# Performance work log

Measured on AMD Instinct MI355X. Metric: run time of the kernel, lower is better.

Reference implementation:

```python
import jax, jax.numpy as jnp
import numpy as np

K = 3          # kernel_size (forced by hardcoded padding=1 in query unfold)
PAD = 1        # padding
C_IN = 64      # conv in_channels (x has C_IN + 5 channels)
C_OUT = 128    # out_channels
B, H, W = 16, 32, 32


def unfold(x, k, pad=0, mode='constant'):
    """torch.nn.functional.unfold equivalent. x: (B,C,H,W) -> (B, C*k*k, L).
    Ordering matches torch: channel slowest, then kernel row, then kernel col."""
    if pad:
        x = jnp.pad(x, ((0, 0), (0, 0), (pad, pad), (pad, pad)), mode=mode)
    b, c, h, w = x.shape
    oh, ow = h - k + 1, w - k + 1
    # (B, C, k*k, oh, ow) with patch index i*k+j
    patches = jnp.stack([x[:, :, i:i + oh, j:j + ow]
                         for i in range(k) for j in range(k)], axis=2)
    return patches.reshape(b, c * k * k, oh * ow)


def conv2d(x, w, b, pad):
    out = jax.lax.conv_general_dilated(
        x, w, window_strides=(1, 1), padding=[(pad, pad), (pad, pad)],
        dimension_numbers=('NCHW', 'OIHW', 'NCHW'))
    return out + b[None, :, None, None]


def setup_inputs() -> dict:
    key = jax.random.key(0)
    ks = jax.random.split(key, 6)
    fan1 = C_IN * K * K
    fan2 = C_OUT * 1 * 1
    return {
        'x': jax.random.normal(ks[0], (B, C_IN + 5, H, W), jnp.float32),
        'conv_w': jax.random.normal(ks[1], (C_OUT, C_IN, K, K), jnp.float32) / np.sqrt(fan1),
        'conv_b': jax.random.normal(ks[2], (C_OUT,), jnp.float32) * 0.01,
        'conv2_w': jax.random.normal(ks[3], (1, C_OUT, 1, 1), jnp.float32) / np.sqrt(fan2),
        'conv2_b': jax.random.normal(ks[4], (1,), jnp.float32) * 0.01,
        'shapes_kernel': jax.random.uniform(ks[5], (1, C_OUT, K * K * 5, 1), jnp.float32),
    }


def reference(x, conv_w, conv_b, conv2_w, conv2_b, shapes_kernel):
    k, pad = K, PAD
    center = k * k // 2

    conv_out = conv2d(x[:, :-5], conv_w, conv_b, pad)          # (B, C_OUT, H', W')
    b, cout, oh, ow = conv_out.shape
    L = oh * ow

    # shape-channel windows (replication-padded), center-relative positions
    sw = unfold(x[:, -5:], k, pad, 'edge').reshape(b, 5, k * k, L)
    sw = sw.at[:, 0:2].add(-sw[:, 0:2, center:center + 1])

    # L1 distance of each window to each learned shape kernel
    sd = jnp.abs(sw.reshape(b, 1, 5 * k * k, L) - shapes_kernel).sum(axis=2)  # (B, C_OUT, L)
    sd = sd.reshape(b, cout, oh, ow)

    saf = jax.nn.relu(conv_out / (sd + 1.0))                    # shape_attended_features

    q = conv2d(saf, conv2_w, conv2_b, 0) / jnp.sqrt(jnp.float32(cout))  # (B, 1, H', W')
    qu = jax.nn.softmax(unfold(q, k, 1), axis=1)[:, None]       # (B, 1, k*k, L), zero-padded

    u_mean = unfold(x[:, -5:-3], k, pad, 'edge').reshape(b, 2, k * k, L)
    means = (u_mean * qu).sum(axis=2)                           # (B, 2, L)

    v1 = (unfold(x[:, -3:-1], k, pad, 'edge').reshape(b, 2, k * k, L) * qu).sum(axis=2)
    v2 = (((u_mean - means[:, :, None, :]) ** 2) * qu).sum(axis=2)
    var = v1 + v2                                               # (B, 2, L)

    c1 = (unfold(x[:, -1:], k, pad, 'edge').reshape(b, 1, k * k, L) * qu).sum(axis=2)
    c2 = ((u_mean[:, 0:1] - means[:, 0:1, None, :]) *
          (u_mean[:, 1:2] - means[:, 1:2, None, :]) * qu).sum(axis=2)
    covar = c1 + c2                                             # (B, 1, L)

    agg = jnp.concatenate([means, var, covar], axis=1).reshape(b, 5, oh, ow)
    return jnp.concatenate([saf, agg], axis=1)                  # (B, C_OUT+5, H', W')
```

## Files before the change

### kernel.cpp

```cpp
#include <hip/hip_runtime.h>
#include <math.h>

#define CI 64
#define CO 128
#define CX 69
#define LPIX 1024

typedef __attribute__((ext_vector_type(8))) short bf16x8;
typedef __attribute__((ext_vector_type(4))) float f32x4;

#define WMF_OFF  0
#define QP_OFF   147456

__device__ __forceinline__ unsigned short f2bf(float f) {
  unsigned u = __float_as_uint(f);
  unsigned r = (u + 0x7fffu + ((u >> 16) & 1u)) >> 16;
  return (unsigned short)r;
}

__launch_bounds__(256)
__global__ void prepW(const float* __restrict__ cwg,
                      unsigned short* __restrict__ wmf) {
  int i = blockIdx.x * 256 + threadIdx.x;
  if (i < 128 * 9 * 64) {
    int co = i / 576, rem = i - co * 576;
    int tap = rem >> 6, ci = rem & 63;
    wmf[i] = f2bf(cwg[co * 576 + ci * 9 + tap]);
  }
}

__launch_bounds__(512, 4)
__global__ void convFused(const float* __restrict__ xg,
                          const unsigned short* __restrict__ wmfg,
                          const float* __restrict__ cbg,
                          const float* __restrict__ w2g,
                          const float* __restrict__ skg,
                          float* __restrict__ qp,
                          float* __restrict__ outg) {
  __shared__ char arena[18432];
  __shared__ float lds_sx[5 * 144];
  __shared__ float qred[8][64];

  unsigned short* ldsB = (unsigned short*)arena;
  float* lds_c = (float*)arena;

  const int tid = threadIdx.x;
  const int blk = blockIdx.x;
  const int coh = blk & 1;
  const int rp  = (blk >> 1) & 15;
  const int b   = blk >> 5;
  const int r0  = rp * 2;

  const int w    = tid >> 6;
  const int lane = tid & 63;
  const int rsel = w >> 2;
  const int ct   = w & 3;
  const int n16  = lane & 15;
  const int kq   = lane >> 4;

  const float* xb = xg + (size_t)b * CX * LPIX;
  const float* xs = xb + CI * LPIX;

  bf16x8 areg[2][9];
  {
    const unsigned short* abase =
        wmfg + (size_t)(coh * 64 + ct * 16 + n16) * 576 + kq * 8;
    #pragma unroll
    for (int ch = 0; ch < 2; ++ch)
      #pragma unroll
      for (int tap = 0; tap < 9; ++tap)
        areg[ch][tap] = *(const bf16x8*)(abase + tap * 64 + ch * 32);
  }

  {
    const int row  = tid >> 7;
    const int cip  = (tid >> 2) & 31;
    const int colq = tid & 3;
    const int ci   = cip * 2;
    const int c0   = colq * 8;
    const int grow = r0 - 1 + row;
    f32x4 u0a = {}, u0b = {}, u1a = {}, u1b = {};
    if ((unsigned)grow < 32u) {
      const float* p0 = xb + ci * LPIX + grow * 32 + c0;
      u0a = *(const f32x4*)p0;          u0b = *(const f32x4*)(p0 + 4);
      u1a = *(const f32x4*)(p0 + LPIX); u1b = *(const f32x4*)(p0 + LPIX + 4);
    }
    #pragma unroll
    for (int cc = 0; cc < 8; ++cc) {
      float f0 = (cc < 4) ? u0a[cc] : u0b[cc - 4];
      float f1 = (cc < 4) ? u1a[cc] : u1b[cc - 4];
      unsigned v = (unsigned)f2bf(f0) | ((unsigned)f2bf(f1) << 16);
      const int slot  = c0 + cc + 1;
      const int gslot = ((ci >> 3) << 3) ^ ((slot & 7) << 3);
      ((unsigned*)ldsB)[(((row * 36 + slot) << 6) + gslot + (ci & 7)) >> 1] = v;
    }
    {
      const int prw = tid >> 7;
      const int s4  = (tid >> 5) & 3;
      const int sl  = (s4 == 0) ? 0 : (32 + s4);
      const int ci2 = (tid & 31) * 2;
      const int gsl = ((ci2 >> 3) << 3) ^ ((sl & 7) << 3);
      ((unsigned*)ldsB)[(((prw * 36 + sl) << 6) + gsl + (ci2 & 7)) >> 1] = 0;
    }
  }

  for (int idx = tid; idx < 5 * 144; idx += 512) {
    int c = idx / 144, rem = idx - c * 144;
    int s = rem / 36, j = rem - s * 36;
    int hh = r0 - 1 + s; hh = hh < 0 ? 0 : (hh > 31 ? 31 : hh);
    int col = j - 1;     col = col < 0 ? 0 : (col > 31 ? 31 : col);
    lds_sx[idx] = xs[c * LPIX + hh * 32 + col];
  }
  __syncthreads();

  f32x4 acc[2] = {};
  #pragma unroll
  for (int tap = 0; tap < 9; ++tap) {
    const int dr = tap / 3, dc = tap % 3;
    const int rowst = rsel + dr;
    #pragma unroll
    for (int ch = 0; ch < 2; ++ch) {
      const int g = (ch << 2) + kq;
      #pragma unroll
      for (int pt = 0; pt < 2; ++pt) {
        const int slot = pt * 16 + n16 + dc;
        const int gs = (g ^ (slot & 7)) << 3;
        bf16x8 bfr = *(const bf16x8*)(ldsB + ((rowst * 36 + slot) << 6) + gs);
        acc[pt] = __builtin_amdgcn_mfma_f32_16x16x32_bf16(areg[ch][tap], bfr,
                                                          acc[pt], 0, 0, 0);
      }
    }
  }
  __syncthreads();

  #pragma unroll
  for (int pt = 0; pt < 2; ++pt) {
    const int pxl = rsel * 32 + pt * 16 + n16;
    const int cog = ct * 4 + kq;
    const int sg  = cog ^ (pxl & 7);
    *(f32x4*)&lds_c[pxl * 64 + sg * 4] = acc[pt];
  }
  __syncthreads();

  const int wS   = __builtin_amdgcn_readfirstlane(w);
  const int co0g = coh * 64 + wS * 8;
  const int pxl  = lane;

  float cvals[8];
  #pragma unroll
  for (int g = 0; g < 2; ++g) {
    const int cog = wS * 2 + g;
    const int sg  = cog ^ (pxl & 7);
    *(f32x4*)&cvals[g * 4] = *(const f32x4*)&lds_c[pxl * 64 + sg * 4];
  }

  const int xbase = (pxl >> 5) * 36 + (pxl & 31);
  float swv[45];
  {
    const float c0 = lds_sx[0 * 144 + 37 + xbase];
    const float c1 = lds_sx[1 * 144 + 37 + xbase];
    #pragma unroll
    for (int c = 0; c < 5; ++c) {
      float ctr = (c == 0) ? c0 : ((c == 1) ? c1 : 0.f);
      #pragma unroll
      for (int s = 0; s < 3; ++s)
        #pragma unroll
        for (int dc = 0; dc < 3; ++dc)
          swv[c * 9 + s * 3 + dc] = lds_sx[c * 144 + s * 36 + dc + xbase] - ctr;
    }
  }

  float sd[8];
  #pragma unroll
  for (int k = 0; k < 8; ++k) {
    const float* kp = skg + (size_t)(co0g + k) * 45;
    float s = 0.f;
    #pragma unroll
    for (int j = 0; j < 45; ++j)
      s += fabsf(swv[j] - kp[j]);
    sd[k] = s;
  }

  float qpv = 0.f;
  float* ob = outg + ((size_t)b * 133 + co0g) * LPIX + (r0 + (pxl >> 5)) * 32 + (pxl & 31);
  #pragma unroll
  for (int k = 0; k < 8; ++k) {
    float v = (cvals[k] + cbg[co0g + k]) * __builtin_amdgcn_rcpf(sd[k] + 1.0f);
    v = v > 0.f ? v : 0.f;
    ob[(size_t)k * LPIX] = v;
    qpv = fmaf(v, w2g[co0g + k], qpv);
  }

  qred[w][lane] = qpv;
  __syncthreads();
  if (tid < 64) {
    float q = 0.f;
    #pragma unroll
    for (int w8 = 0; w8 < 8; ++w8) q += qred[w8][tid];
    qp[coh * 16384 + b * LPIX + r0 * 32 + tid] = q;
  }
}

__launch_bounds__(64)
__global__ void statsB(const float* __restrict__ xg,
                       const float* __restrict__ qp,
                       const float* __restrict__ b2g,
                       float* __restrict__ outg) {
  const int gid = blockIdx.x * 64 + threadIdx.x;
  const int b = gid >> 10;
  const int h = (gid >> 5) & 31;
  const int w = gid & 31;

  const float b2 = b2g[0];
  const float* q0 = qp + (size_t)b * LPIX;
  float qv[9];
  float m = -1e30f;
  #pragma unroll
  for (int t = 0; t < 9; ++t) {
    int hh = h + t / 3 - 1, wc = w + t % 3 - 1;
    float v = 0.f;
    if ((unsigned)hh < 32u && (unsigned)wc < 32u) {
      int off = hh * 32 + wc;
      v = (q0[off] + q0[16384 + off] + b2) * 0.08838834764831845f;
    }
    qv[t] = v;
    m = fmaxf(m, v);
  }
  float ssum = 0.f;
  #pragma unroll
  for (int t = 0; t < 9; ++t) { qv[t] = expf(qv[t] - m); ssum += qv[t]; }
  const float inv = 1.f / ssum;

  const float* xs = xg + ((size_t)b * CX + CI) * LPIX;
  float um0[9], um1[9];
  float m0 = 0.f, m1 = 0.f, v1a = 0.f, v1b = 0.f, c1 = 0.f;
  #pragma unroll
  for (int t = 0; t < 9; ++t) {
    int hh = h + t / 3 - 1; hh = hh < 0 ? 0 : (hh > 31 ? 31 : hh);
    int wc = w + t % 3 - 1; wc = wc < 0 ? 0 : (wc > 31 ? 31 : wc);
    int off = hh * 32 + wc;
    float quv = qv[t] * inv;
    qv[t] = quv;
    float a0 = xs[off];
    float a1 = xs[LPIX + off];
    float b0 = xs[2 * LPIX + off];
    float b1 = xs[3 * LPIX + off];
    float cc = xs[4 * LPIX + off];
    um0[t] = a0; um1[t] = a1;
    m0 = fmaf(a0, quv, m0);
    m1 = fmaf(a1, quv, m1);
    v1a = fmaf(b0, quv, v1a);
    v1b = fmaf(b1, quv, v1b);
    c1 = fmaf(cc, quv, c1);
  }
  float var0 = v1a, var1 = v1b, cov = c1;
  #pragma unroll
  for (int t = 0; t < 9; ++t) {
    float d0 = um0[t] - m0, d1 = um1[t] - m1;
    var0 = fmaf(d0 * d0, qv[t], var0);
    var1 = fmaf(d1 * d1, qv[t], var1);
    cov  = fmaf(d0 * d1, qv[t], cov);
  }
  float* ob = outg + ((size_t)b * 133 + 128) * LPIX + h * 32 + w;
  ob[0 * LPIX] = m0;
  ob[1 * LPIX] = m1;
  ob[2 * LPIX] = var0;
  ob[3 * LPIX] = var1;
  ob[4 * LPIX] = cov;
}

extern "C" void kernel_launch(void* const* d_in, const int* in_sizes, int n_in,
                              void* d_out, int out_size, void* d_ws, size_t ws_size,
                              hipStream_t stream) {
  const float* x  = (const float*)d_in[0];
  const float* cw = (const float*)d_in[1];
  const float* cb = (const float*)d_in[2];
  const float* w2 = (const float*)d_in[3];
  const float* b2 = (const float*)d_in[4];
  const float* sk = (const float*)d_in[5];
  float* out = (float*)d_out;

  unsigned short* wmf = (unsigned short*)((char*)d_ws + WMF_OFF);
  float* qp = (float*)((char*)d_ws + QP_OFF);

  prepW<<<dim3(576), dim3(256), 0, stream>>>(cw, wmf);
  convFused<<<dim3(512), dim3(512), 0, stream>>>(x, wmf, cb, w2, sk, qp, out);
  statsB<<<dim3(256), dim3(64), 0, stream>>>(x, qp, b2, out);
}
```

Baseline: 29.64 us.

## Compute all output channels per block in fused conv with 1024 threads

```diff
diff --git a/kernel.cpp b/kernel.cpp
--- a/kernel.cpp
+++ b/kernel.cpp
@@ -29,7 +29,7 @@
   }
 }
 
-__launch_bounds__(512, 4)
+__launch_bounds__(1024, 4)
 __global__ void convFused(const float* __restrict__ xg,
                           const unsigned short* __restrict__ wmfg,
                           const float* __restrict__ cbg,
@@ -37,24 +37,23 @@
                           const float* __restrict__ skg,
                           float* __restrict__ qp,
                           float* __restrict__ outg) {
-  __shared__ char arena[18432];
+  __shared__ char arena[32768];
   __shared__ float lds_sx[5 * 144];
-  __shared__ float qred[8][64];
+  __shared__ float qred[16][64];
 
   unsigned short* ldsB = (unsigned short*)arena;
   float* lds_c = (float*)arena;
 
   const int tid = threadIdx.x;
   const int blk = blockIdx.x;
-  const int coh = blk & 1;
-  const int rp  = (blk >> 1) & 15;
-  const int b   = blk >> 5;
+  const int rp  = blk & 15;
+  const int b   = blk >> 4;
   const int r0  = rp * 2;
 
   const int w    = tid >> 6;
   const int lane = tid & 63;
-  const int rsel = w >> 2;
-  const int ct   = w & 3;
+  const int rsel = w >> 3;
+  const int ct   = w & 7;
   const int n16  = lane & 15;
   const int kq   = lane >> 4;
 
@@ -64,7 +63,7 @@
   bf16x8 areg[2][9];
   {
     const unsigned short* abase =
-        wmfg + (size_t)(coh * 64 + ct * 16 + n16) * 576 + kq * 8;
+        wmfg + (size_t)(ct * 16 + n16) * 576 + kq * 8;
     #pragma unroll
     for (int ch = 0; ch < 2; ++ch)
       #pragma unroll
@@ -73,28 +72,27 @@
   }
 
   {
-    const int row  = tid >> 7;
-    const int cip  = (tid >> 2) & 31;
-    const int colq = tid & 3;
+    const int row  = tid >> 8;
+    const int rem  = tid & 255;
+    const int cip  = rem >> 3;
+    const int colq = rem & 7;
     const int ci   = cip * 2;
-    const int c0   = colq * 8;
+    const int c0   = colq * 4;
     const int grow = r0 - 1 + row;
-    f32x4 u0a = {}, u0b = {}, u1a = {}, u1b = {};
+    f32x4 u0 = {}, u1 = {};
     if ((unsigned)grow < 32u) {
       const float* p0 = xb + ci * LPIX + grow * 32 + c0;
-      u0a = *(const f32x4*)p0;          u0b = *(const f32x4*)(p0 + 4);
-      u1a = *(const f32x4*)(p0 + LPIX); u1b = *(const f32x4*)(p0 + LPIX + 4);
-    }
-    #pragma unroll
-    for (int cc = 0; cc < 8; ++cc) {
-      float f0 = (cc < 4) ? u0a[cc] : u0b[cc - 4];
-      float f1 = (cc < 4) ? u1a[cc] : u1b[cc - 4];
-      unsigned v = (unsigned)f2bf(f0) | ((unsigned)f2bf(f1) << 16);
+      u0 = *(const f32x4*)p0;
+      u1 = *(const f32x4*)(p0 + LPIX);
+    }
+    #pragma unroll
+    for (int cc = 0; cc < 4; ++cc) {
+      unsigned v = (unsigned)f2bf(u0[cc]) | ((unsigned)f2bf(u1[cc]) << 16);
       const int slot  = c0 + cc + 1;
       const int gslot = ((ci >> 3) << 3) ^ ((slot & 7) << 3);
       ((unsigned*)ldsB)[(((row * 36 + slot) << 6) + gslot + (ci & 7)) >> 1] = v;
     }
-    {
+    if (tid < 512) {
       const int prw = tid >> 7;
       const int s4  = (tid >> 5) & 3;
       const int sl  = (s4 == 0) ? 0 : (32 + s4);
@@ -104,12 +102,12 @@
     }
   }
 
-  for (int idx = tid; idx < 5 * 144; idx += 512) {
-    int c = idx / 144, rem = idx - c * 144;
+  if (tid < 5 * 144) {
+    int c = tid / 144, rem = tid - c * 144;
     int s = rem / 36, j = rem - s * 36;
     int hh = r0 - 1 + s; hh = hh < 0 ? 0 : (hh > 31 ? 31 : hh);
     int col = j - 1;     col = col < 0 ? 0 : (col > 31 ? 31 : col);
-    lds_sx[idx] = xs[c * LPIX + hh * 32 + col];
+    lds_sx[tid] = xs[c * LPIX + hh * 32 + col];
   }
   __syncthreads();
 
@@ -138,12 +136,12 @@
     const int pxl = rsel * 32 + pt * 16 + n16;
     const int cog = ct * 4 + kq;
     const int sg  = cog ^ (pxl & 7);
-    *(f32x4*)&lds_c[pxl * 64 + sg * 4] = acc[pt];
+    *(f32x4*)&lds_c[pxl * 128 + sg * 4] = acc[pt];
   }
   __syncthreads();
 
   const int wS   = __builtin_amdgcn_readfirstlane(w);
-  const int co0g = coh * 64 + wS * 8;
+  const int co0g = wS * 8;
   const int pxl  = lane;
 
   float cvals[8];
@@ -151,7 +149,7 @@
   for (int g = 0; g < 2; ++g) {
     const int cog = wS * 2 + g;
     const int sg  = cog ^ (pxl & 7);
-    *(f32x4*)&cvals[g * 4] = *(const f32x4*)&lds_c[pxl * 64 + sg * 4];
+    *(f32x4*)&cvals[g * 4] = *(const f32x4*)&lds_c[pxl * 128 + sg * 4];
   }
 
   const int xbase = (pxl >> 5) * 36 + (pxl & 31);
@@ -196,8 +194,8 @@
   if (tid < 64) {
     float q = 0.f;
     #pragma unroll
-    for (int w8 = 0; w8 < 8; ++w8) q += qred[w8][tid];
-    qp[coh * 16384 + b * LPIX + r0 * 32 + tid] = q;
+    for (int w16 = 0; w16 < 16; ++w16) q += qred[w16][tid];
+    qp[b * LPIX + r0 * 32 + tid] = q;
   }
 }
 
@@ -221,7 +219,7 @@
     float v = 0.f;
     if ((unsigned)hh < 32u && (unsigned)wc < 32u) {
       int off = hh * 32 + wc;
-      v = (q0[off] + q0[16384 + off] + b2) * 0.08838834764831845f;
+      v = (q0[off] + b2) * 0.08838834764831845f;
     }
     qv[t] = v;
     m = fmaxf(m, v);
@@ -283,7 +281,7 @@
   unsigned short* wmf = (unsigned short*)((char*)d_ws + WMF_OFF);
   float* qp = (float*)((char*)d_ws + QP_OFF);
 
-  prepW<<<dim3(576), dim3(256), 0, stream>>>(cw, wmf);
-  convFused<<<dim3(512), dim3(512), 0, stream>>>(x, wmf, cb, w2, sk, qp, out);
+  prepW<<<dim3(288), dim3(256), 0, stream>>>(cw, wmf);
+  convFused<<<dim3(256), dim3(1024), 0, stream>>>(x, wmf, cb, w2, sk, qp, out);
   statsB<<<dim3(256), dim3(64), 0, stream>>>(x, qp, b2, out);
 }
```

Result: slower. 30.51 us (+2.9%).
